# Kernel tuning notes

Hardware: AMD Instinct MI355X
Metric: run time of the kernel (lower is better)

The kernel has to match this reference:

```python
import jax, jax.numpy as jnp
import numpy as np

B = 256      # graph pairs
N = 256      # nodes per graph (uniform -> padding is a reshape)
DEG = 16     # avg degree
D = 32       # one_hot_dim
F1, F2, F3 = 128, 64, 64
T = 16       # tensor_neurons
BINS = 16
BOT = 16     # bottle_neck_neurons


def setup_inputs() -> dict:
    key = jax.random.key(0)
    ks = jax.random.split(key, 24)
    NT = B * N            # total nodes per side
    NE = B * N * DEG      # total directed edges per side
    x_q = jax.random.normal(ks[0], (NT, D), jnp.float32)
    x_c = jax.random.normal(ks[1], (NT, D), jnp.float32)
    edge_q = jax.random.randint(ks[2], (2, NE), 0, NT, jnp.int32)
    edge_c = jax.random.randint(ks[3], (2, NE), 0, NT, jnp.int32)
    qgraph_sizes = jnp.full((B,), N, jnp.int32)
    cgraph_sizes = jnp.full((B,), N, jnp.int32)

    def glorot(k, shape):
        fan = sum(shape[-2:]) if len(shape) >= 2 else shape[0] * 2
        return jax.random.uniform(k, shape, jnp.float32, -1.0, 1.0) * np.sqrt(6.0 / fan)

    params = dict(
        W1=glorot(ks[4], (D, F1)), b1=jnp.zeros((F1,), jnp.float32),
        W2=glorot(ks[5], (F1, F2)), b2=jnp.zeros((F2,), jnp.float32),
        W3=glorot(ks[6], (F2, F3)), b3=jnp.zeros((F3,), jnp.float32),
        attn_w=glorot(ks[7], (F3, F3)),
        ntn_a_w=glorot(ks[8], (T, F3, F3)),
        ntn_b_w=glorot(ks[9], (2 * F3, T)),
        ntn_bias=glorot(ks[10], (T, 1)),
        fc1_w=glorot(ks[11], (T + BINS, BOT)), fc1_b=jnp.zeros((BOT,), jnp.float32),
        fc2_w=glorot(ks[12], (BOT, 1)), fc2_b=jnp.zeros((1,), jnp.float32),
    )
    return dict(x_q=x_q, edge_q=edge_q, x_c=x_c, edge_c=edge_c,
                qgraph_sizes=qgraph_sizes, cgraph_sizes=cgraph_sizes, **params)


def _gcn(x, src, dst, W, b):
    n = x.shape[0]
    h = x @ W
    loop = jnp.arange(n, dtype=src.dtype)
    s = jnp.concatenate([src, loop])
    d = jnp.concatenate([dst, loop])
    deg = jax.ops.segment_sum(jnp.ones(s.shape, h.dtype), d, num_segments=n)
    dinv = jnp.where(deg > 0, jax.lax.rsqrt(jnp.maximum(deg, 1.0)), 0.0)
    coef = (dinv[s] * dinv[d])[:, None]
    return jax.ops.segment_sum(h[s] * coef, d, num_segments=n) + b


def _gnn(x, ei, W1, b1, W2, b2, W3, b3):
    src, dst = ei[0], ei[1]
    h = jax.nn.relu(_gcn(x, src, dst, W1, b1))        # dropout is identity in eval
    h = jax.nn.relu(_gcn(h, src, dst, W2, b2))
    return _gcn(h, src, dst, W3, b3)                  # [B*N, F3]


def _att_pool(q, attn_w, sizes):
    # q: [B, N, F3]
    ctx = jnp.tanh((q.sum(axis=1) @ attn_w) / sizes.astype(q.dtype)[:, None])  # [B, F3]
    sig = jax.nn.sigmoid(jnp.einsum('bnf,bf->bn', q, ctx))                      # [B, N]
    return jnp.einsum('bnf,bn->bf', q, sig)                                     # [B, F3]


def _pair_hist(q, c):
    # per-pair histogram of q @ c^T with BINS bins over each pair's [min, max]
    s = jax.lax.stop_gradient(jnp.einsum('bnf,bmf->bnm', q, c))  # [B, N, N]
    mn = s.min(axis=(1, 2), keepdims=True)
    mx = s.max(axis=(1, 2), keepdims=True)
    idx = jnp.clip(jnp.floor((s - mn) / jnp.maximum(mx - mn, 1e-12) * BINS),
                   0, BINS - 1).astype(jnp.int32)
    gid = (idx + jnp.arange(B, dtype=jnp.int32)[:, None, None] * BINS).reshape(-1)
    h = jax.ops.segment_sum(jnp.ones(gid.shape, jnp.float32), gid,
                            num_segments=B * BINS).reshape(B, BINS)
    return h / h.sum(axis=1, keepdims=True)


def reference(x_q, edge_q, x_c, edge_c, qgraph_sizes, cgraph_sizes,
              W1, b1, W2, b2, W3, b3, attn_w, ntn_a_w, ntn_b_w, ntn_bias,
              fc1_w, fc1_b, fc2_w, fc2_b):
    q = _gnn(x_q, edge_q, W1, b1, W2, b2, W3, b3).reshape(B, N, F3)
    c = _gnn(x_c, edge_c, W1, b1, W2, b2, W3, b3).reshape(B, N, F3)
    e1 = _att_pool(q, attn_w, qgraph_sizes)
    e2 = _att_pool(c, attn_w, cgraph_sizes)
    ntn = (jnp.einsum('bi,tij,bj->bt', e1, ntn_a_w, e2)
           + jnp.concatenate([e1, e2], axis=-1) @ ntn_b_w
           + ntn_bias[:, 0])
    scores = jax.nn.relu(ntn)                                   # [B, T]
    hist = _pair_hist(q, c)                                     # [B, BINS]
    scores = jnp.concatenate([scores, hist], axis=1)
    scores = jax.nn.relu(scores @ fc1_w + fc1_b)
    p = jax.nn.sigmoid(scores @ fc2_w + fc2_b)[:, 0]            # [B]
    ged = -0.5 * (qgraph_sizes + cgraph_sizes).astype(p.dtype) * jnp.log(p)
    return ged
```

## Files before the change

kernel.cpp:

```cpp
#include <hip/hip_runtime.h>
#include <hip/hip_bf16.h>
#include <math.h>

#define BB 256
#define NN 256
#define NT (BB*NN)
#define NT2 (2*NT)
#define NE (NT*16)
#define DD 32
#define F1C 128
#define F2C 64
#define F3C 64
#define TT 16
#define BINS 16

#define NBUCK 256
#define BSHIFT 9
#define BNODES 512
#define BCAP 10240
#define EPB 4096

typedef __attribute__((ext_vector_type(8))) short short8;
typedef __attribute__((ext_vector_type(4))) float f32x4;

__device__ inline float b2f(ushort u) { return __uint_as_float(((uint)u) << 16); }
__device__ inline ushort f2b(float f) {
    uint u = __float_as_uint(f);
    return (ushort)((u + 0x7fffu + ((u >> 16) & 1u)) >> 16);
}

__global__ __launch_bounds__(256) void prep_k(const float* __restrict__ W1, const float* __restrict__ W2,
                                              const float* __restrict__ W3, ushort* __restrict__ Wt1,
                                              ushort* __restrict__ Wt2, ushort* __restrict__ Wt3,
                                              int* __restrict__ gcount) {
    int i = blockIdx.x * 256 + threadIdx.x;
    if (i < NBUCK) gcount[i] = 0;
    if (i < DD * F1C)  { int k = i / F1C, n = i % F1C; Wt1[n * DD + k]  = f2b(W1[i]); }
    if (i < F1C * F2C) { int k = i / F2C, n = i % F2C; Wt2[n * F1C + k] = f2b(W2[i]); }
    if (i < F2C * F3C) { int k = i / F3C, n = i % F3C; Wt3[n * F2C + k] = f2b(W3[i]); }
}

__global__ __launch_bounds__(256) void csr_p1_k(const int* __restrict__ eq, const int* __restrict__ ec,
                                                uint* __restrict__ staged, int* __restrict__ gcount) {
    __shared__ uint s_pk[EPB];
    __shared__ int s_cnt[NBUCK];
    __shared__ int s_off[NBUCK];
    __shared__ int s_base[NBUCK];
    __shared__ int s_gb[NBUCK];
    int t = threadIdx.x;
    bool sideB = blockIdx.x >= 256;
    const int* edge = sideB ? ec : eq;
    int off = sideB ? NT : 0;
    int e0 = (blockIdx.x & 255) * EPB;
    s_cnt[t] = 0;
    __syncthreads();
    uint pk[16]; int bk[16];
#pragma unroll
    for (int j = 0; j < 16; j++) {
        int e = e0 + j * 256 + t;
        int s = edge[e] + off;
        int d = edge[NE + e] + off;
        bk[j] = d >> BSHIFT;
        pk[j] = ((uint)s << BSHIFT) | (uint)(d & (BNODES - 1));
        atomicAdd(&s_cnt[bk[j]], 1);
    }
    __syncthreads();
    s_off[t] = s_cnt[t];
    __syncthreads();
    for (int o = 1; o < NBUCK; o <<= 1) {
        int x = (t >= o) ? s_off[t - o] : 0;
        __syncthreads();
        s_off[t] += x;
        __syncthreads();
    }
    {
        int ex = s_off[t] - s_cnt[t];
        s_base[t] = ex;
        s_off[t] = ex;
        s_gb[t] = atomicAdd(&gcount[t], s_cnt[t]);
    }
    __syncthreads();
#pragma unroll
    for (int j = 0; j < 16; j++) {
        int pos = atomicAdd(&s_off[bk[j]], 1);
        s_pk[pos] = pk[j];
    }
    __syncthreads();
    int w = t >> 6, l = t & 63;
    int bsel = l >> 4, l16 = l & 15;
    for (int pb = w; pb < NBUCK / 4; pb += 4) {
        int b = pb * 4 + bsel;
        int n = s_cnt[b], st = s_base[b], gb = s_gb[b];
        if (gb + n > BCAP) n = max(0, BCAP - gb);
        for (int i = l16; i < n; i += 16)
            staged[b * BCAP + gb + i] = s_pk[st + i];
    }
}

__global__ __launch_bounds__(256) void csr_p2_k(const uint* __restrict__ staged, const int* __restrict__ gcount,
                                                int* __restrict__ rp, int* __restrict__ indeg,
                                                float* __restrict__ dinv, int* __restrict__ ep) {
    int b = blockIdx.x;
    int t = threadIdx.x;
    __shared__ int cnt[BNODES];
    __shared__ int fl[BNODES];
    __shared__ int wsum[256];
    __shared__ int gsc[NBUCK];
    cnt[t] = 0; cnt[t + 256] = 0;
    gsc[t] = min(gcount[t], BCAP);
    __syncthreads();
    for (int off = 1; off < NBUCK; off <<= 1) {
        int x = (t >= off) ? gsc[t - off] : 0;
        __syncthreads();
        gsc[t] += x;
        __syncthreads();
    }
    int gbase = (b == 0) ? 0 : gsc[b - 1];
    int n = min(gcount[b], BCAP);
    const uint* sb = staged + (size_t)b * BCAP;
    int i = t;
    for (; i + 768 < n; i += 1024) {
        uint p0 = sb[i];
        uint p1 = sb[i + 256];
        uint p2 = sb[i + 512];
        uint p3 = sb[i + 768];
        atomicAdd(&cnt[p0 & (BNODES - 1)], 1);
        atomicAdd(&cnt[p1 & (BNODES - 1)], 1);
        atomicAdd(&cnt[p2 & (BNODES - 1)], 1);
        atomicAdd(&cnt[p3 & (BNODES - 1)], 1);
    }
    for (; i < n; i += 256)
        atomicAdd(&cnt[sb[i] & (BNODES - 1)], 1);
    __syncthreads();
    int base2 = t * 2;
    int c0 = cnt[base2], c1 = cnt[base2 + 1];
    int s2 = c0 + c1;
    wsum[t] = s2;
    __syncthreads();
    for (int off = 1; off < 256; off <<= 1) {
        int x = (t >= off) ? wsum[t - off] : 0;
        __syncthreads();
        wsum[t] += x;
        __syncthreads();
    }
    int p = gbase + wsum[t] - s2;
    int v0 = b * BNODES + base2;
    rp[v0] = p;          fl[base2] = p;
    indeg[v0] = c0;      dinv[v0] = rsqrtf((float)(c0 + 1));
    p += c0;
    rp[v0 + 1] = p;      fl[base2 + 1] = p;
    indeg[v0 + 1] = c1;  dinv[v0 + 1] = rsqrtf((float)(c1 + 1));
    __syncthreads();
    i = t;
    for (; i + 768 < n; i += 1024) {
        uint p0 = sb[i];
        uint p1 = sb[i + 256];
        uint p2 = sb[i + 512];
        uint p3 = sb[i + 768];
        ep[atomicAdd(&fl[p0 & (BNODES - 1)], 1)] = (int)(p0 >> BSHIFT);
        ep[atomicAdd(&fl[p1 & (BNODES - 1)], 1)] = (int)(p1 >> BSHIFT);
        ep[atomicAdd(&fl[p2 & (BNODES - 1)], 1)] = (int)(p2 >> BSHIFT);
        ep[atomicAdd(&fl[p3 & (BNODES - 1)], 1)] = (int)(p3 >> BSHIFT);
    }
    for (; i < n; i += 256) {
        uint pk = sb[i];
        ep[atomicAdd(&fl[pk & (BNODES - 1)], 1)] = (int)(pk >> BSHIFT);
    }
}

__global__ __launch_bounds__(256) void cvt2_k(const float* __restrict__ a, const float* __restrict__ b,
                                              const float* __restrict__ dinv, ushort* __restrict__ out) {
    int i = blockIdx.x * 256 + threadIdx.x;
    const int per = NT * DD / 4;
    bool sideB = i >= per;
    const float4* src = (const float4*)(sideB ? b : a);
    float4 v = src[sideB ? i - per : i];
    float dv = dinv[i / (DD / 4)];
    ushort4 o;
    o.x = f2b(v.x * dv); o.y = f2b(v.y * dv); o.z = f2b(v.z * dv); o.w = f2b(v.w * dv);
    ((ushort4*)out)[i] = o;
}

template<int F, bool BIAS, bool RELU>
__global__ __launch_bounds__(256) void agg_bf_k(const ushort* __restrict__ in, const int* __restrict__ rp,
                                                const int* __restrict__ indeg, const int* __restrict__ ep,
                                                const float* __restrict__ dinv,
                                                const float* __restrict__ bias, ushort* __restrict__ out) {
    constexpr int LPV = F / 8;
    constexpr int VPB = 256 / LPV;
    int g = threadIdx.x / LPV;
    int l = threadIdx.x % LPV;
    int v = blockIdx.x * VPB + g;
    float dv = dinv[v];
    short8 rs = *(const short8*)(in + (size_t)v * F + l * 8);
    float acc[8];
#pragma unroll
    for (int j = 0; j < 8; j++) acc[j] = b2f((ushort)rs[j]);
    int start = rp[v];
    int cnt   = indeg[v];
    int i = 0;
    for (; i + 4 <= cnt; i += 4) {
        int s0 = ep[start + i];
        int s1 = ep[start + i + 1];
        int s2 = ep[start + i + 2];
        int s3 = ep[start + i + 3];
        short8 r0 = *(const short8*)(in + (size_t)s0 * F + l * 8);
        short8 r1 = *(const short8*)(in + (size_t)s1 * F + l * 8);
        short8 r2 = *(const short8*)(in + (size_t)s2 * F + l * 8);
        short8 r3 = *(const short8*)(in + (size_t)s3 * F + l * 8);
#pragma unroll
        for (int j = 0; j < 8; j++) {
            acc[j] += b2f((ushort)r0[j]);
            acc[j] += b2f((ushort)r1[j]);
            acc[j] += b2f((ushort)r2[j]);
            acc[j] += b2f((ushort)r3[j]);
        }
    }
    for (; i < cnt; i++) {
        int s0 = ep[start + i];
        short8 r0 = *(const short8*)(in + (size_t)s0 * F + l * 8);
#pragma unroll
        for (int j = 0; j < 8; j++) acc[j] += b2f((ushort)r0[j]);
    }
    short8 o;
#pragma unroll
    for (int j = 0; j < 8; j++) {
        float x = dv * acc[j];
        if (BIAS) x += bias[l * 8 + j];
        if (RELU) x = fmaxf(x, 0.0f);
        o[j] = (short)f2b(x);
    }
    *(short8*)(out + (size_t)v * F + l * 8) = o;
}

template<int K, int N, bool BIAS, bool RELU, bool SCALE>
__global__ __launch_bounds__(256) void gemm_mfma_k(const ushort* __restrict__ A,
                                                   const ushort* __restrict__ Wt,
                                                   const float* __restrict__ bias,
                                                   const float* __restrict__ dinv,
                                                   ushort* __restrict__ out) {
    constexpr int KC = K / 32;
    int w = threadIdx.x >> 6, lane = threadIdx.x & 63;
    int r16 = lane & 15, koff = (lane >> 4) * 8;
    size_t rows0 = (size_t)blockIdx.x * 128;

    short8 af[KC][2];
#pragma unroll
    for (int kc = 0; kc < KC; kc++)
#pragma unroll
        for (int mt = 0; mt < 2; mt++)
            af[kc][mt] = *(const short8*)(A + (rows0 + (w * 2 + mt) * 16 + r16) * K + kc * 32 + koff);

    float dvr[2][4];
#pragma unroll
    for (int mt = 0; mt < 2; mt++)
#pragma unroll
        for (int r = 0; r < 4; r++)
            dvr[mt][r] = SCALE ? dinv[rows0 + (w * 2 + mt) * 16 + (lane >> 4) * 4 + r] : 1.0f;

#pragma unroll
    for (int nt = 0; nt < N / 16; nt++) {
        f32x4 acc[2] = {{0.f,0.f,0.f,0.f},{0.f,0.f,0.f,0.f}};
#pragma unroll
        for (int kc = 0; kc < KC; kc++) {
            short8 b = *(const short8*)(Wt + (size_t)(nt * 16 + r16) * K + kc * 32 + koff);
            acc[0] = __builtin_amdgcn_mfma_f32_16x16x32_bf16(af[kc][0], b, acc[0], 0, 0, 0);
            acc[1] = __builtin_amdgcn_mfma_f32_16x16x32_bf16(af[kc][1], b, acc[1], 0, 0, 0);
        }
#pragma unroll
        for (int mt = 0; mt < 2; mt++) {
#pragma unroll
            for (int r = 0; r < 4; r++) {
                size_t row = rows0 + (w * 2 + mt) * 16 + (lane >> 4) * 4 + r;
                int col = nt * 16 + (lane & 15);
                float v = acc[mt][r];
                if (BIAS) v += bias[col];
                if (RELU) v = fmaxf(v, 0.0f);
                if (SCALE) v *= dvr[mt][r];
                out[row * N + col] = f2b(v);
            }
        }
    }
}

__global__ __launch_bounds__(256) void pool_k(const ushort* __restrict__ fin,
                                              const int* __restrict__ qsz, const int* __restrict__ csz,
                                              const float* __restrict__ attn_w, float* __restrict__ e_out) {
    int b = blockIdx.x & 255;
    bool is_c = blockIdx.x >= BB;
    const ushort* emb = fin + (size_t)blockIdx.x * NN * F3C;
    float size = (float)((is_c ? csz : qsz)[b]);
    float* eo = e_out + (is_c ? BB * F3C : 0) + b * F3C;

    int t = threadIdx.x;
    int f = t & 63;
    int w = t >> 6;

    __shared__ float s_emb[NN][F3C + 1];
    __shared__ float s_red[4][64];
    __shared__ float s_sq[64];
    __shared__ float s_ctx[64];
    __shared__ float s_sig[NN];

    float psum = 0.0f;
    for (int n = w; n < NN; n += 4) {
        float v = b2f(emb[n * F3C + f]);
        s_emb[n][f] = v;
        psum += v;
    }
    s_red[w][f] = psum;
    __syncthreads();

    if (w == 0) {
        s_sq[f] = s_red[0][f] + s_red[1][f] + s_red[2][f] + s_red[3][f];
        float acc = 0.0f;
        for (int k = 0; k < 64; k++) acc += s_sq[k] * attn_w[k * 64 + f];
        s_ctx[f] = tanhf(acc / size);
    }
    __syncthreads();

    {
        float acc = 0.0f;
#pragma unroll 8
        for (int k = 0; k < 64; k++) acc += s_emb[t][k] * s_ctx[k];
        s_sig[t] = 1.0f / (1.0f + expf(-acc));
    }
    __syncthreads();

    float eacc = 0.0f;
#pragma unroll 8
    for (int i = 0; i < 64; i++) {
        int n = w * 64 + i;
        eacc += s_sig[n] * s_emb[n][f];
    }
    s_red[w][f] = eacc;
    __syncthreads();
    if (w == 0) eo[f] = s_red[0][f] + s_red[1][f] + s_red[2][f] + s_red[3][f];
}

__global__ __launch_bounds__(256) void hist_k(const ushort* __restrict__ qbf, const ushort* __restrict__ cbf,
                                              float* __restrict__ histp) {
    int b = blockIdx.x;
    const ushort* qb = qbf + (size_t)b * NN * 64;
    const ushort* cb = cbf + (size_t)b * NN * 64;
    int lane = threadIdx.x & 63;
    int w = threadIdx.x >> 6;
    int r16 = lane & 15, koff = (lane >> 4) * 8;

    short8 a[4][2];
#pragma unroll
    for (int i = 0; i < 4; i++) {
        int row = (w * 4 + i) * 16 + r16;
#pragma unroll
        for (int kk = 0; kk < 2; kk++)
            a[i][kk] = *(const short8*)(qb + row * 64 + kk * 32 + koff);
    }

    float mn = 1e30f, mx = -1e30f;
    for (int mt = 0; mt < 16; mt++) {
        int crow = mt * 16 + r16;
        short8 b0 = *(const short8*)(cb + crow * 64 + koff);
        short8 b1 = *(const short8*)(cb + crow * 64 + 32 + koff);
#pragma unroll
        for (int i = 0; i < 4; i++) {
            f32x4 acc = {0.0f, 0.0f, 0.0f, 0.0f};
            acc = __builtin_amdgcn_mfma_f32_16x16x32_bf16(a[i][0], b0, acc, 0, 0, 0);
            acc = __builtin_amdgcn_mfma_f32_16x16x32_bf16(a[i][1], b1, acc, 0, 0, 0);
            mn = fminf(mn, fminf(fminf(acc[0], acc[1]), fminf(acc[2], acc[3])));
            mx = fmaxf(mx, fmaxf(fmaxf(acc[0], acc[1]), fmaxf(acc[2], acc[3])));
        }
    }
    for (int off = 32; off; off >>= 1) {
        mn = fminf(mn, __shfl_xor(mn, off, 64));
        mx = fmaxf(mx, __shfl_xor(mx, off, 64));
    }
    __shared__ float smn[4], smx[4];
    __shared__ float s_mn, s_scale;
    if (lane == 0) { smn[w] = mn; smx[w] = mx; }
    __syncthreads();
    if (threadIdx.x == 0) {
        float m0 = fminf(fminf(smn[0], smn[1]), fminf(smn[2], smn[3]));
        float m1 = fmaxf(fmaxf(smx[0], smx[1]), fmaxf(smx[2], smx[3]));
        s_mn = m0;
        s_scale = 16.0f / fmaxf(m1 - m0, 1e-12f);
    }
    __shared__ int h[16 * 256];
#pragma unroll
    for (int i = 0; i < 16; i++) h[i * 256 + threadIdx.x] = 0;
    __syncthreads();
    float bmn = s_mn, bscale = s_scale;

    for (int mt = 0; mt < 16; mt++) {
        int crow = mt * 16 + r16;
        short8 b0 = *(const short8*)(cb + crow * 64 + koff);
        short8 b1 = *(const short8*)(cb + crow * 64 + 32 + koff);
#pragma unroll
        for (int i = 0; i < 4; i++) {
            f32x4 acc = {0.0f, 0.0f, 0.0f, 0.0f};
            acc = __builtin_amdgcn_mfma_f32_16x16x32_bf16(a[i][0], b0, acc, 0, 0, 0);
            acc = __builtin_amdgcn_mfma_f32_16x16x32_bf16(a[i][1], b1, acc, 0, 0, 0);
#pragma unroll
            for (int r = 0; r < 4; r++) {
                int bin = (int)floorf((acc[r] - bmn) * bscale);
                bin = min(max(bin, 0), 15);
                h[bin * 256 + threadIdx.x] += 1;
            }
        }
    }
    __syncthreads();
    __shared__ int hp[16][16];
    int bb = threadIdx.x >> 4, part = threadIdx.x & 15;
    int sum = 0;
#pragma unroll
    for (int j = 0; j < 16; j++) sum += h[bb * 256 + part * 16 + j];
    hp[bb][part] = sum;
    __syncthreads();
    if (threadIdx.x < 16) {
        int s = 0;
#pragma unroll
        for (int j = 0; j < 16; j++) s += hp[threadIdx.x][j];
        histp[b * 16 + threadIdx.x] = (float)s;
    }
}

__global__ __launch_bounds__(256) void ntn_final_k(const float* __restrict__ e, const float* __restrict__ A,
                                                   const float* __restrict__ bw, const float* __restrict__ bias,
                                                   const float* __restrict__ histp,
                                                   const float* __restrict__ fc1w, const float* __restrict__ fc1b,
                                                   const float* __restrict__ fc2w, const float* __restrict__ fc2b,
                                                   const int* __restrict__ qsz, const int* __restrict__ csz,
                                                   float* __restrict__ out) {
    int b = blockIdx.x;
    int t = threadIdx.x;
    __shared__ float s_e1[64], s_e2[64];
    __shared__ float s_ntn[16];
    __shared__ float s_s[32];
    __shared__ float s_a[16];
    if (t < 64) s_e1[t] = e[b * 64 + t];
    else if (t < 128) s_e2[t - 64] = e[BB * 64 + b * 64 + (t - 64)];
    if (t < 16) s_ntn[t] = 0.0f;
    __syncthreads();
#pragma unroll
    for (int r = 0; r < 4; r++) {
        int idx = t + r * 256;
        int tt = idx >> 6, i = idx & 63;
        const float* Ar = A + (size_t)idx * 64;
        float acc = 0.0f;
        for (int j = 0; j < 64; j++) acc += Ar[j] * s_e2[j];
        atomicAdd(&s_ntn[tt], s_e1[i] * acc);
    }
    __syncthreads();
    if (t < 16) {
        float acc = s_ntn[t] + bias[t];
        for (int k = 0; k < 64; k++) acc += s_e1[k] * bw[k * 16 + t];
        for (int k = 0; k < 64; k++) acc += s_e2[k] * bw[(64 + k) * 16 + t];
        s_s[t] = fmaxf(acc, 0.0f);
        s_s[16 + t] = histp[b * 16 + t] * (1.0f / 65536.0f);
    }
    __syncthreads();
    if (t < 16) {
        float a = fc1b[t];
        for (int k = 0; k < 32; k++) a += s_s[k] * fc1w[k * 16 + t];
        s_a[t] = fmaxf(a, 0.0f);
    }
    __syncthreads();
    if (t == 0) {
        float z = fc2b[0];
        for (int j = 0; j < 16; j++) z += s_a[j] * fc2w[j];
        float nz = -z;
        float sp = (nz > 20.0f) ? nz : log1pf(expf(nz));
        out[b] = 0.5f * (float)(qsz[b] + csz[b]) * sp;
    }
}

extern "C" void kernel_launch(void* const* d_in, const int* in_sizes, int n_in,
                              void* d_out, int out_size, void* d_ws, size_t ws_size,
                              hipStream_t stream) {
    const float* x_q    = (const float*)d_in[0];
    const int*   edge_q = (const int*)d_in[1];
    const float* x_c    = (const float*)d_in[2];
    const int*   edge_c = (const int*)d_in[3];
    const int*   qsz    = (const int*)d_in[4];
    const int*   csz    = (const int*)d_in[5];
    const float* W1 = (const float*)d_in[6];
    const float* b1 = (const float*)d_in[7];
    const float* W2 = (const float*)d_in[8];
    const float* b2 = (const float*)d_in[9];
    const float* W3 = (const float*)d_in[10];
    const float* b3 = (const float*)d_in[11];
    const float* attn_w  = (const float*)d_in[12];
    const float* ntn_a   = (const float*)d_in[13];
    const float* ntn_b   = (const float*)d_in[14];
    const float* ntn_bias= (const float*)d_in[15];
    const float* fc1w = (const float*)d_in[16];
    const float* fc1b = (const float*)d_in[17];
    const float* fc2w = (const float*)d_in[18];
    const float* fc2b = (const float*)d_in[19];
    float* out = (float*)d_out;

    char* w = (char*)d_ws;
    auto alloc = [&](size_t bytes) -> void* {
        void* p = (void*)w;
        w += (bytes + 255) & ~(size_t)255;
        return p;
    };
    int*    rp     = (int*)alloc((size_t)NT2 * 4);
    int*    indeg  = (int*)alloc((size_t)NT2 * 4);
    float*  dinv   = (float*)alloc((size_t)NT2 * 4);
    int*    gcount = (int*)alloc(NBUCK * 4);
    uint*   staged = (uint*)alloc((size_t)NBUCK * BCAP * 4);
    int*    ep     = (int*)alloc((size_t)2 * NE * 4);
    ushort* xb     = (ushort*)alloc((size_t)NT2 * 32 * 2);
    ushort* xa     = (ushort*)alloc((size_t)NT2 * 32 * 2);
    ushort* hA     = (ushort*)alloc((size_t)NT2 * 128 * 2);
    ushort* hB     = (ushort*)alloc((size_t)NT2 * 64 * 2);
    ushort* hC     = (ushort*)alloc((size_t)NT2 * 64 * 2);
    ushort* fin    = (ushort*)alloc((size_t)NT2 * 64 * 2);
    ushort* Wt1    = (ushort*)alloc((size_t)DD * F1C * 2);
    ushort* Wt2    = (ushort*)alloc((size_t)F1C * F2C * 2);
    ushort* Wt3    = (ushort*)alloc((size_t)F2C * F3C * 2);
    float*  e12    = (float*)alloc(2 * BB * 64 * 4);
    float*  histp  = (float*)alloc(256 * 16 * 4);
    ushort* qfin = fin;
    ushort* cfin = fin + (size_t)NT * 64;

    prep_k<<<32, 256, 0, stream>>>(W1, W2, W3, Wt1, Wt2, Wt3, gcount);
    csr_p1_k<<<512, 256, 0, stream>>>(edge_q, edge_c, staged, gcount);
    csr_p2_k<<<NBUCK, 256, 0, stream>>>(staged, gcount, rp, indeg, dinv, ep);

    cvt2_k<<<NT2 * 32 / 4 / 256, 256, 0, stream>>>(x_q, x_c, dinv, xb);

    agg_bf_k<32, false, false><<<NT2 / 64, 256, 0, stream>>>(xb, rp, indeg, ep, dinv, nullptr, xa);
    gemm_mfma_k<32, 128, true, true, false><<<NT2 / 128, 256, 0, stream>>>(xa, Wt1, b1, nullptr, hA);
    gemm_mfma_k<128, 64, false, false, true><<<NT2 / 128, 256, 0, stream>>>(hA, Wt2, nullptr, dinv, hB);
    agg_bf_k<64, true, true><<<NT2 / 32, 256, 0, stream>>>(hB, rp, indeg, ep, dinv, b2, hC);
    gemm_mfma_k<64, 64, false, false, true><<<NT2 / 128, 256, 0, stream>>>(hC, Wt3, nullptr, dinv, hB);
    agg_bf_k<64, true, false><<<NT2 / 32, 256, 0, stream>>>(hB, rp, indeg, ep, dinv, b3, fin);

    pool_k<<<2 * BB, 256, 0, stream>>>(fin, qsz, csz, attn_w, e12);
    hist_k<<<BB, 256, 0, stream>>>(qfin, cfin, histp);
    ntn_final_k<<<BB, 256, 0, stream>>>(e12, ntn_a, ntn_b, ntn_bias, histp,
                                        fc1w, fc1b, fc2w, fc2b, qsz, csz, out);
}
```

Measured before the change: 336.0 us.

## Store layer-2/3 intermediate activations in FP8 for gathers and GEMM

```diff
diff --git a/kernel.cpp b/kernel.cpp
--- a/kernel.cpp
+++ b/kernel.cpp
@@ -22,22 +22,43 @@
 
 typedef __attribute__((ext_vector_type(8))) short short8;
 typedef __attribute__((ext_vector_type(4))) float f32x4;
+typedef __attribute__((ext_vector_type(2))) float f32x2;
 
 __device__ inline float b2f(ushort u) { return __uint_as_float(((uint)u) << 16); }
 __device__ inline ushort f2b(float f) {
     uint u = __float_as_uint(f);
     return (ushort)((u + 0x7fffu + ((u >> 16) & 1u)) >> 16);
 }
+__device__ inline float clamp8(float v) { return fminf(fmaxf(v, -448.0f), 448.0f); }
+__device__ inline uchar f2f8(float v) {
+    int r = __builtin_amdgcn_cvt_pk_fp8_f32(clamp8(v), 0.0f, 0, false);
+    return (uchar)(r & 0xff);
+}
+__device__ inline void f8x8_acc(uint2 w, float* acc) {
+    f32x2 p;
+    p = __builtin_amdgcn_cvt_pk_f32_fp8(w.x, false); acc[0] += p.x; acc[1] += p.y;
+    p = __builtin_amdgcn_cvt_pk_f32_fp8(w.x, true);  acc[2] += p.x; acc[3] += p.y;
+    p = __builtin_amdgcn_cvt_pk_f32_fp8(w.y, false); acc[4] += p.x; acc[5] += p.y;
+    p = __builtin_amdgcn_cvt_pk_f32_fp8(w.y, true);  acc[6] += p.x; acc[7] += p.y;
+}
+__device__ inline uint2 f8x8_pack(const float* v) {
+    uint2 r;
+    r.x = (uint)__builtin_amdgcn_cvt_pk_fp8_f32(clamp8(v[0]), clamp8(v[1]), 0, false);
+    r.x = (uint)__builtin_amdgcn_cvt_pk_fp8_f32(clamp8(v[2]), clamp8(v[3]), (int)r.x, true);
+    r.y = (uint)__builtin_amdgcn_cvt_pk_fp8_f32(clamp8(v[4]), clamp8(v[5]), 0, false);
+    r.y = (uint)__builtin_amdgcn_cvt_pk_fp8_f32(clamp8(v[6]), clamp8(v[7]), (int)r.y, true);
+    return r;
+}
 
 __global__ __launch_bounds__(256) void prep_k(const float* __restrict__ W1, const float* __restrict__ W2,
                                               const float* __restrict__ W3, ushort* __restrict__ Wt1,
-                                              ushort* __restrict__ Wt2, ushort* __restrict__ Wt3,
+                                              ushort* __restrict__ Wt2, uchar* __restrict__ Wt3f8,
                                               int* __restrict__ gcount) {
     int i = blockIdx.x * 256 + threadIdx.x;
     if (i < NBUCK) gcount[i] = 0;
     if (i < DD * F1C)  { int k = i / F1C, n = i % F1C; Wt1[n * DD + k]  = f2b(W1[i]); }
     if (i < F1C * F2C) { int k = i / F2C, n = i % F2C; Wt2[n * F1C + k] = f2b(W2[i]); }
-    if (i < F2C * F3C) { int k = i / F3C, n = i % F3C; Wt3[n * F2C + k] = f2b(W3[i]); }
+    if (i < F2C * F3C) { int k = i / F3C, n = i % F3C; Wt3f8[n * F2C + k] = f2f8(W3[i]); }
 }
 
 __global__ __launch_bounds__(256) void csr_p1_k(const int* __restrict__ eq, const int* __restrict__ ec,
@@ -233,12 +254,58 @@
     *(short8*)(out + (size_t)v * F + l * 8) = o;
 }
 
-template<int K, int N, bool BIAS, bool RELU, bool SCALE>
+template<bool OUT_BF16, bool BIAS, bool RELU>
+__global__ __launch_bounds__(256) void agg_f8_k(const uchar* __restrict__ in, const int* __restrict__ rp,
+                                                const int* __restrict__ indeg, const int* __restrict__ ep,
+                                                const float* __restrict__ dinv,
+                                                const float* __restrict__ bias, void* __restrict__ outp) {
+    int g = threadIdx.x >> 3;
+    int l = threadIdx.x & 7;
+    int v = blockIdx.x * 32 + g;
+    float dv = dinv[v];
+    float acc[8] = {0, 0, 0, 0, 0, 0, 0, 0};
+    f8x8_acc(*(const uint2*)(in + (size_t)v * 64 + l * 8), acc);
+    int start = rp[v];
+    int cnt   = indeg[v];
+    int i = 0;
+    for (; i + 4 <= cnt; i += 4) {
+        int s0 = ep[start + i];
+        int s1 = ep[start + i + 1];
+        int s2 = ep[start + i + 2];
+        int s3 = ep[start + i + 3];
+        uint2 g0 = *(const uint2*)(in + (size_t)s0 * 64 + l * 8);
+        uint2 g1 = *(const uint2*)(in + (size_t)s1 * 64 + l * 8);
+        uint2 g2 = *(const uint2*)(in + (size_t)s2 * 64 + l * 8);
+        uint2 g3 = *(const uint2*)(in + (size_t)s3 * 64 + l * 8);
+        f8x8_acc(g0, acc); f8x8_acc(g1, acc); f8x8_acc(g2, acc); f8x8_acc(g3, acc);
+    }
+    for (; i < cnt; i++) {
+        int s0 = ep[start + i];
+        f8x8_acc(*(const uint2*)(in + (size_t)s0 * 64 + l * 8), acc);
+    }
+#pragma unroll
+    for (int j = 0; j < 8; j++) {
+        float x = dv * acc[j];
+        if (BIAS) x += bias[l * 8 + j];
+        if (RELU) x = fmaxf(x, 0.0f);
+        acc[j] = x;
+    }
+    if (OUT_BF16) {
+        short8 o;
+#pragma unroll
+        for (int j = 0; j < 8; j++) o[j] = (short)f2b(acc[j]);
+        *(short8*)((ushort*)outp + (size_t)v * 64 + l * 8) = o;
+    } else {
+        *(uint2*)((uchar*)outp + (size_t)v * 64 + l * 8) = f8x8_pack(acc);
+    }
+}
+
+template<int K, int N, bool BIAS, bool RELU, bool SCALE, bool OUT8>
 __global__ __launch_bounds__(256) void gemm_mfma_k(const ushort* __restrict__ A,
                                                    const ushort* __restrict__ Wt,
                                                    const float* __restrict__ bias,
                                                    const float* __restrict__ dinv,
-                                                   ushort* __restrict__ out) {
+                                                   void* __restrict__ outp) {
     constexpr int KC = K / 32;
     int w = threadIdx.x >> 6, lane = threadIdx.x & 63;
     int r16 = lane & 15, koff = (lane >> 4) * 8;
@@ -277,7 +344,51 @@
                 if (BIAS) v += bias[col];
                 if (RELU) v = fmaxf(v, 0.0f);
                 if (SCALE) v *= dvr[mt][r];
-                out[row * N + col] = f2b(v);
+                if (OUT8) ((uchar*)outp)[row * N + col] = f2f8(v);
+                else      ((ushort*)outp)[row * N + col] = f2b(v);
+            }
+        }
+    }
+}
+
+__global__ __launch_bounds__(256) void gemm_f8_k(const uchar* __restrict__ A8,
+                                                 const uchar* __restrict__ Wt8,
+                                                 const float* __restrict__ dinv,
+                                                 uchar* __restrict__ out8) {
+    int w = threadIdx.x >> 6, lane = threadIdx.x & 63;
+    int r16 = lane & 15, koff = (lane >> 4) * 8;
+    size_t rows0 = (size_t)blockIdx.x * 128;
+
+    long af[2][2];
+#pragma unroll
+    for (int kc = 0; kc < 2; kc++)
+#pragma unroll
+        for (int mt = 0; mt < 2; mt++)
+            af[kc][mt] = *(const long*)(A8 + (rows0 + (w * 2 + mt) * 16 + r16) * 64 + kc * 32 + koff);
+
+    float dvr[2][4];
+#pragma unroll
+    for (int mt = 0; mt < 2; mt++)
+#pragma unroll
+        for (int r = 0; r < 4; r++)
+            dvr[mt][r] = dinv[rows0 + (w * 2 + mt) * 16 + (lane >> 4) * 4 + r];
+
+#pragma unroll
+    for (int nt = 0; nt < 4; nt++) {
+        f32x4 acc[2] = {{0.f,0.f,0.f,0.f},{0.f,0.f,0.f,0.f}};
+#pragma unroll
+        for (int kc = 0; kc < 2; kc++) {
+            long b = *(const long*)(Wt8 + (size_t)(nt * 16 + r16) * 64 + kc * 32 + koff);
+            acc[0] = __builtin_amdgcn_mfma_f32_16x16x32_fp8_fp8(af[kc][0], b, acc[0], 0, 0, 0);
+            acc[1] = __builtin_amdgcn_mfma_f32_16x16x32_fp8_fp8(af[kc][1], b, acc[1], 0, 0, 0);
+        }
+#pragma unroll
+        for (int mt = 0; mt < 2; mt++) {
+#pragma unroll
+            for (int r = 0; r < 4; r++) {
+                size_t row = rows0 + (w * 2 + mt) * 16 + (lane >> 4) * 4 + r;
+                int col = nt * 16 + (lane & 15);
+                out8[row * 64 + col] = f2f8(acc[mt][r] * dvr[mt][r]);
             }
         }
     }
@@ -513,29 +624,29 @@
     ushort* xb     = (ushort*)alloc((size_t)NT2 * 32 * 2);
     ushort* xa     = (ushort*)alloc((size_t)NT2 * 32 * 2);
     ushort* hA     = (ushort*)alloc((size_t)NT2 * 128 * 2);
-    ushort* hB     = (ushort*)alloc((size_t)NT2 * 64 * 2);
-    ushort* hC     = (ushort*)alloc((size_t)NT2 * 64 * 2);
+    uchar*  h8a    = (uchar*)alloc((size_t)NT2 * 64);
+    uchar*  h8b    = (uchar*)alloc((size_t)NT2 * 64);
     ushort* fin    = (ushort*)alloc((size_t)NT2 * 64 * 2);
     ushort* Wt1    = (ushort*)alloc((size_t)DD * F1C * 2);
     ushort* Wt2    = (ushort*)alloc((size_t)F1C * F2C * 2);
-    ushort* Wt3    = (ushort*)alloc((size_t)F2C * F3C * 2);
+    uchar*  Wt3f8  = (uchar*)alloc((size_t)F2C * F3C);
     float*  e12    = (float*)alloc(2 * BB * 64 * 4);
     float*  histp  = (float*)alloc(256 * 16 * 4);
     ushort* qfin = fin;
     ushort* cfin = fin + (size_t)NT * 64;
 
-    prep_k<<<32, 256, 0, stream>>>(W1, W2, W3, Wt1, Wt2, Wt3, gcount);
+    prep_k<<<32, 256, 0, stream>>>(W1, W2, W3, Wt1, Wt2, Wt3f8, gcount);
     csr_p1_k<<<512, 256, 0, stream>>>(edge_q, edge_c, staged, gcount);
     csr_p2_k<<<NBUCK, 256, 0, stream>>>(staged, gcount, rp, indeg, dinv, ep);
 
     cvt2_k<<<NT2 * 32 / 4 / 256, 256, 0, stream>>>(x_q, x_c, dinv, xb);
 
     agg_bf_k<32, false, false><<<NT2 / 64, 256, 0, stream>>>(xb, rp, indeg, ep, dinv, nullptr, xa);
-    gemm_mfma_k<32, 128, true, true, false><<<NT2 / 128, 256, 0, stream>>>(xa, Wt1, b1, nullptr, hA);
-    gemm_mfma_k<128, 64, false, false, true><<<NT2 / 128, 256, 0, stream>>>(hA, Wt2, nullptr, dinv, hB);
-    agg_bf_k<64, true, true><<<NT2 / 32, 256, 0, stream>>>(hB, rp, indeg, ep, dinv, b2, hC);
-    gemm_mfma_k<64, 64, false, false, true><<<NT2 / 128, 256, 0, stream>>>(hC, Wt3, nullptr, dinv, hB);
-    agg_bf_k<64, true, false><<<NT2 / 32, 256, 0, stream>>>(hB, rp, indeg, ep, dinv, b3, fin);
+    gemm_mfma_k<32, 128, true, true, false, false><<<NT2 / 128, 256, 0, stream>>>(xa, Wt1, b1, nullptr, hA);
+    gemm_mfma_k<128, 64, false, false, true, true><<<NT2 / 128, 256, 0, stream>>>(hA, Wt2, nullptr, dinv, h8a);
+    agg_f8_k<false, true, true><<<NT2 / 32, 256, 0, stream>>>(h8a, rp, indeg, ep, dinv, b2, h8b);
+    gemm_f8_k<<<NT2 / 128, 256, 0, stream>>>(h8b, Wt3f8, dinv, h8a);
+    agg_f8_k<true, true, false><<<NT2 / 32, 256, 0, stream>>>(h8a, rp, indeg, ep, dinv, b3, fin);
 
     pool_k<<<2 * BB, 256, 0, stream>>>(fin, qsz, csz, attn_w, e12);
     hist_k<<<BB, 256, 0, stream>>>(qfin, cfin, histp);
```

Result: faster. 319.4 us (-5.0%).
